# Optimization experiments

Hardware: AMD Instinct MI355X
Metric: run time of the kernel (lower is better)

Reference implementation:

```python
import jax, jax.numpy as jnp
import numpy as np

B, S, HIDDEN = 2, 4096, 4096
NUM_HEADS = 32
QK_NOPE = 128
QK_ROPE = 64
QK_HEAD = QK_NOPE + QK_ROPE
KV_LORA = 512
Q_LORA = 1536


def setup_inputs() -> dict:
    key = jax.random.key(0)
    k1, k2, k3, k4, k5, k6 = jax.random.split(key, 6)
    x = jax.random.normal(k1, (B, S, HIDDEN), dtype=jnp.float32)
    cos = jax.random.uniform(k2, (B, S, QK_ROPE), dtype=jnp.float32)
    sin = jax.random.uniform(k3, (B, S, QK_ROPE), dtype=jnp.float32)
    # Linear weights, torch layout [out, in]
    Wqa = jax.random.normal(k4, (Q_LORA, HIDDEN), dtype=jnp.float32) * 0.02
    Wqb = jax.random.normal(k5, (NUM_HEADS * QK_HEAD, Q_LORA), dtype=jnp.float32) * 0.02
    Wkva = jax.random.normal(k6, (KV_LORA + QK_ROPE, HIDDEN), dtype=jnp.float32) * 0.02
    return {"x": x, "cos": cos, "sin": sin, "Wqa": Wqa, "Wqb": Wqb, "Wkva": Wkva}


def _rotate_half(t):
    d = t.shape[-1] // 2
    return jnp.concatenate([-t[..., d:], t[..., :d]], axis=-1)


def reference(x, cos, sin, Wqa, Wqb, Wkva):
    b, s, _ = x.shape
    # low-rank Q: x -> q_lora -> heads*(nope+rope)
    q = jnp.einsum('bsh,rh->bsr', x, Wqa)
    q = jnp.einsum('bsr,or->bso', q, Wqb).reshape(b, s, NUM_HEADS, QK_HEAD)
    q_nope = q[..., :QK_NOPE]
    q_pe = q[..., QK_NOPE:]
    # KV down-projection with MQA rope part
    kv = jnp.einsum('bsh,oh->bso', x, Wkva)
    compressed_kv = kv[..., :KV_LORA]                         # [b,s,kv_lora]
    k_pe = kv[..., KV_LORA:].reshape(b, s, 1, QK_ROPE)
    # NeoX explicit RoPE, unsqueeze_dim=2
    c = cos[:, :, None, :]
    sn = sin[:, :, None, :]
    q_pe_rot = q_pe * c + _rotate_half(q_pe) * sn
    k_pe_rot = k_pe * c + _rotate_half(k_pe) * sn
    q_out = jnp.concatenate([q_nope, q_pe_rot], axis=-1).reshape(b, s, -1)
    k_out = k_pe_rot.reshape(b, s, QK_ROPE)
    return jnp.concatenate([q_out, k_out, compressed_kv], axis=-1)
```

## Files before the change

### kernel.cpp

```cpp
#include <hip/hip_runtime.h>
#include <hip/hip_bf16.h>
#include <stdint.h>

typedef __bf16 bf16x8 __attribute__((ext_vector_type(8)));
typedef float f32x4 __attribute__((ext_vector_type(4)));
typedef float fvec4 __attribute__((ext_vector_type(4)));
typedef unsigned short usvec4 __attribute__((ext_vector_type(4)));
typedef unsigned int ui32x4 __attribute__((ext_vector_type(4)));

#define AS3 __attribute__((address_space(3)))
#define AS1 __attribute__((address_space(1)))

static __device__ __forceinline__ unsigned short f2bf(float f) {
  unsigned int u = __float_as_uint(f);
  u += 0x7FFF + ((u >> 16) & 1);
  return (unsigned short)(u >> 16);
}


extern "C" __global__ void cvt_bf16_kernel(const float* __restrict__ src,
                                           unsigned short* __restrict__ dst,
                                           long n4) {
  long i = (long)blockIdx.x * blockDim.x + threadIdx.x;
  const long stride = (long)gridDim.x * blockDim.x;
  for (; i < n4; i += stride) {
    const fvec4 v = __builtin_nontemporal_load(&((const fvec4*)src)[i]);
    usvec4 o;
    o.x = f2bf(v.x); o.y = f2bf(v.y); o.z = f2bf(v.z); o.w = f2bf(v.w);
    ((usvec4*)dst)[i] = o;
  }
}

extern "C" __global__ void cvt_pad_kernel(const float* __restrict__ src,
                                          unsigned short* __restrict__ dst,
                                          long nsrc4, long ntot4) {
  long i = (long)blockIdx.x * blockDim.x + threadIdx.x;
  const long stride = (long)gridDim.x * blockDim.x;
  for (; i < ntot4; i += stride) {
    usvec4 o = {0, 0, 0, 0};
    if (i < nsrc4) {
      const fvec4 v = __builtin_nontemporal_load(&((const fvec4*)src)[i]);
      o.x = f2bf(v.x); o.y = f2bf(v.y); o.z = f2bf(v.z); o.w = f2bf(v.w);
    }
    ((usvec4*)dst)[i] = o;
  }
}

#define VMW(N) asm volatile("s_waitcnt vmcnt(" #N ")" ::: "memory")
#define BAR() do { __builtin_amdgcn_s_barrier(); \
                   __builtin_amdgcn_sched_barrier(0); } while (0)
#define LGKM0() do { asm volatile("s_waitcnt lgkmcnt(0)" ::: "memory"); \
                     __builtin_amdgcn_sched_barrier(0); } while (0)


template <int MODE>
__global__ __launch_bounds__(512, 2)
void mla_gemm(const __hip_bfloat16* __restrict__ A0p,
              const __hip_bfloat16* __restrict__ B0p, int K0,
              unsigned short* __restrict__ qlora,
              const float* __restrict__ cosp,
              const float* __restrict__ sinp,
              float* __restrict__ out) {
  extern __shared__ __align__(128) char lds[];
  const int tid = threadIdx.x;
  const int lane = tid & 63;
  const int w = tid >> 6;
  const int wm = w >> 2, wn = w & 3;
  const int l15 = lane & 15, lhi = lane >> 4;
  const int srow8 = lane >> 3;
  const int swzc = ((lane & 7) ^ srow8) * 8;

  const int bm = (int)blockIdx.x >> 3;
  const int bn = (int)blockIdx.x & 7;
  const __hip_bfloat16* Aptr = A0p;
  const __hip_bfloat16* Bptr = B0p;
  const int K = K0;
  const long brow = (long)bm * 256;
  const int bcol = bn * 256;

  const __hip_bfloat16* aSt = Aptr + (brow + w * 16 + srow8) * (long)K + swzc;
  const __hip_bfloat16* bSt = Bptr + ((long)bcol + srow8) * (long)K + swzc;
  const int wj0 = w * 16, wj1 = w * 16 + 8;
  const int cb_j0 = (2 * (wj0 >> 5)) * 32 + (wj0 & 31);
  const int cb_j1 = (2 * (wj1 >> 5)) * 32 + (wj1 & 31);
  const int ldsWj = w * 2048;

  const int aRdRow = (wm * 64 + l15) * 128;
  const int bRdRow = (wn * 32 + l15) * 128;
  const int ck0 = (lhi ^ (l15 & 7)) * 16;

  f32x4 acc[8][4] = {};
  bf16x8 aF[4][2];
  bf16x8 bF[2][2][2];

  const int T = K >> 6;

  auto stage = [&](int u, int kt) {
    const int b = kt & 1;
    if (u < 2) {
      const int off = b * 32768 + u * 16384 + ldsWj;
      __builtin_amdgcn_global_load_lds((AS1 void*)(aSt + (long)(u * 128) * K + kt * 64),
                                       (AS3 void*)(lds + off), 16, 0, 0);
      __builtin_amdgcn_global_load_lds((AS1 void*)(aSt + (long)(u * 128 + 8) * K + kt * 64),
                                       (AS3 void*)(lds + off + 1024), 16, 0, 0);
    } else {
      const int h = u - 2;
      const int off = 65536 + b * 32768 + h * 16384 + ldsWj;
      __builtin_amdgcn_global_load_lds((AS1 void*)(bSt + (long)(cb_j0 + h * 32) * K + kt * 64),
                                       (AS3 void*)(lds + off), 16, 0, 0);
      __builtin_amdgcn_global_load_lds((AS1 void*)(bSt + (long)(cb_j1 + h * 32) * K + kt * 64),
                                       (AS3 void*)(lds + off + 1024), 16, 0, 0);
    }
  };
  auto readA = [&](int qh, int b) {
    const int base = b * 32768 + qh * 16384 + aRdRow;
    #pragma unroll
    for (int fr = 0; fr < 4; ++fr) {
      aF[fr][0] = *(const bf16x8*)(lds + base + fr * 2048 + ck0);
      aF[fr][1] = *(const bf16x8*)(lds + base + fr * 2048 + (ck0 ^ 64));
    }
  };
  auto readB = [&](int c, int b) {
    const int base = 65536 + b * 32768 + c * 16384 + bRdRow;
    #pragma unroll
    for (int fq = 0; fq < 2; ++fq) {
      bF[c][fq][0] = *(const bf16x8*)(lds + base + fq * 2048 + ck0);
      bF[c][fq][1] = *(const bf16x8*)(lds + base + fq * 2048 + (ck0 ^ 64));
    }
  };
  auto mmac = [&](int qh, int c) {
    __builtin_amdgcn_s_setprio(1);
    #pragma unroll
    for (int fr = 0; fr < 4; ++fr)
      #pragma unroll
      for (int fq = 0; fq < 2; ++fq) {
        acc[qh * 4 + fr][c * 2 + fq] = __builtin_amdgcn_mfma_f32_16x16x32_bf16(
            aF[fr][0], bF[c][fq][0], acc[qh * 4 + fr][c * 2 + fq], 0, 0, 0);
        acc[qh * 4 + fr][c * 2 + fq] = __builtin_amdgcn_mfma_f32_16x16x32_bf16(
            aF[fr][1], bF[c][fq][1], acc[qh * 4 + fr][c * 2 + fq], 0, 0, 0);
      }
    __builtin_amdgcn_s_setprio(0);
  };

  stage(0, 0); stage(2, 0); stage(3, 0); stage(1, 0);
  stage(0, 1); stage(2, 1); stage(3, 1); stage(1, 1);
  VMW(12);
  BAR();

  for (int t = 0; t < T - 2; ++t) {
    const int b = t & 1;
    readA(0, b); readB(0, b); if (t) stage(1, t + 1);
    VMW(10); BAR(); LGKM0(); mmac(0, 0);
    readB(1, b);
    VMW(8); BAR(); LGKM0(); mmac(0, 1);
    readA(1, b); stage(0, t + 2); stage(2, t + 2);
    BAR(); LGKM0(); mmac(1, 1);
    stage(3, t + 2);
    VMW(10); BAR(); mmac(1, 0);
  }
  {
    const int b = (T - 2) & 1;
    readA(0, b); readB(0, b); stage(1, T - 1);
    VMW(10); BAR(); LGKM0(); mmac(0, 0);
    readB(1, b);
    VMW(8); BAR(); LGKM0(); mmac(0, 1);
    readA(1, b);
    BAR(); LGKM0(); mmac(1, 1);
    VMW(4); BAR(); mmac(1, 0);
  }
  {
    const int b = (T - 1) & 1;
    readA(0, b); readB(0, b);
    VMW(2); BAR(); LGKM0(); mmac(0, 0);
    readB(1, b);
    VMW(0); BAR(); LGKM0(); mmac(0, 1);
    readA(1, b);
    BAR(); LGKM0(); mmac(1, 1);
    BAR(); mmac(1, 0);
  }

  const int wcol = bcol + wn * 64;
  const long rbase = brow + wm * 64;
  char* eplds = lds + w * 4096;

  auto storeTileF32 = [&](int i8, float* dst) {
    #pragma unroll
    for (int j = 0; j < 4; ++j)
      #pragma unroll
      for (int r = 0; r < 4; ++r)
        *(float*)(eplds + (lhi * 4 + r) * 256 + ((j >> 1) * 32 + (j & 1) * 16 + l15) * 4) =
            acc[i8][j][r];
    asm volatile("s_waitcnt lgkmcnt(0)" ::: "memory");
    #pragma unroll
    for (int t = 0; t < 4; ++t) {
      const int r16 = t * 4 + (lane >> 4);
      const f32x4 v = *(const f32x4*)(eplds + r16 * 256 + (lane & 15) * 16);
      const long row = rbase + (i8 >> 2) * 128 + (i8 & 3) * 16 + r16;
      __builtin_nontemporal_store(v, (f32x4*)(dst + row * 6720 + (lane & 15) * 4));
    }
  };
  auto storeTileBf16 = [&](int i8) {
    #pragma unroll
    for (int j = 0; j < 4; ++j)
      #pragma unroll
      for (int r = 0; r < 4; ++r)
        *(unsigned short*)(eplds + (lhi * 4 + r) * 128 +
                           ((j >> 1) * 32 + (j & 1) * 16 + l15) * 2) = f2bf(acc[i8][j][r]);
    asm volatile("s_waitcnt lgkmcnt(0)" ::: "memory");
    #pragma unroll
    for (int t = 0; t < 2; ++t) {
      const int r16 = t * 8 + (lane >> 3);
      const ui32x4 v = *(const ui32x4*)(eplds + r16 * 128 + (lane & 7) * 16);
      const long row = rbase + (i8 >> 2) * 128 + (i8 & 3) * 16 + r16;
      *(ui32x4*)((char*)qlora + (row * 1536 + wcol) * 2 + (lane & 7) * 16) = v;
    }
  };

  if (wcol < 1536) {
    #pragma unroll
    for (int i8 = 0; i8 < 8; ++i8) storeTileBf16(i8);
  } else {
    #pragma unroll
    for (int i8 = 0; i8 < 8; ++i8) storeTileF32(i8, out + wcol + 4672);
  }
}


__global__ __launch_bounds__(512, 4)
void mla_gemm2(const __hip_bfloat16* __restrict__ Aq,
               const __hip_bfloat16* __restrict__ Bq,
               const __hip_bfloat16* __restrict__ Ak,
               const __hip_bfloat16* __restrict__ Bk,
               const float* __restrict__ cosp,
               const float* __restrict__ sinp,
               float* __restrict__ out) {
  extern __shared__ __align__(128) char lds[];
  const int tid = threadIdx.x;
  const int lane = tid & 63;
  const int w = tid >> 6;
  const int wm = w >> 1, wn = w & 1;
  const int l15 = lane & 15, lhi = lane >> 4;
  const int srow = lane >> 2;
  const int sslot = (lane & 3) ^ ((lane >> 3) & 3);

  const __hip_bfloat16* Ap;
  const __hip_bfloat16* Bp;
  int K, bm, bn;
  bool kpe;
  const int bid = (int)blockIdx.x;
  if (bid < 32) {
    kpe = true; bm = bid; bn = 0; Ap = Ak; Bp = Bk; K = 4096;
  } else {
    kpe = false;
    const int b2 = bid - 32;
    const int x = b2 & 7;
    const int i = b2 >> 3;
    const int r6 = i % 6;
    bm = i / 6;
    bn = x * 6 + r6;
    Ap = Aq; Bp = Bq; K = 1536;
  }
  const long brow = (long)bm * 256;
  const int bcol = bn * 128;

  const __hip_bfloat16* aSt = Ap + (brow + w * 16 + srow) * (long)K + sslot * 8;
  const __hip_bfloat16* bSt = Bp + ((long)bcol + w * 16 + srow) * (long)K + sslot * 8;

  const int kslot = (lhi ^ ((l15 >> 1) & 3)) * 16;
  const int aRd = (wm * 64 + l15) * 64 + kslot;
  const int bRd = 16384 + (wn * 64 + l15) * 64 + kslot;

  f32x4 acc[4][4] = {};
  const int T = K >> 5;

  auto stage = [&](int kt, int buf) {
    const int bo = buf * 24576;
    __builtin_amdgcn_global_load_lds((AS1 void*)(aSt + (long)kt * 32),
                                     (AS3 void*)(lds + bo + w * 1024), 16, 0, 0);
    __builtin_amdgcn_global_load_lds((AS1 void*)(aSt + 128L * K + (long)kt * 32),
                                     (AS3 void*)(lds + bo + 8192 + w * 1024), 16, 0, 0);
    __builtin_amdgcn_global_load_lds((AS1 void*)(bSt + (long)kt * 32),
                                     (AS3 void*)(lds + bo + 16384 + w * 1024), 16, 0, 0);
  };

  stage(0, 0); stage(1, 1);
  VMW(3);
  BAR();

  int cur = 0;
  for (int t = 0; t < T; ++t) {
    const int bo = cur * 24576;
    bf16x8 aF[4], bF[4];
    #pragma unroll
    for (int f = 0; f < 4; ++f)
      aF[f] = *(const bf16x8*)(lds + bo + aRd + f * 1024);
    #pragma unroll
    for (int f = 0; f < 4; ++f)
      bF[f] = *(const bf16x8*)(lds + bo + bRd + f * 1024);
    if (t + 2 < T) {
      int nx = cur + 2; if (nx >= 3) nx -= 3;
      stage(t + 2, nx);
      VMW(3);
    } else if (t + 2 == T) {
      VMW(0);
    }
    LGKM0();
    if (t < T - 1) BAR();
    __builtin_amdgcn_s_setprio(1);
    #pragma unroll
    for (int fr = 0; fr < 4; ++fr)
      #pragma unroll
      for (int fc = 0; fc < 4; ++fc)
        acc[fr][fc] = __builtin_amdgcn_mfma_f32_16x16x32_bf16(
            aF[fr], bF[fc], acc[fr][fc], 0, 0, 0);
    __builtin_amdgcn_s_setprio(0);
    cur = cur + 1; if (cur == 3) cur = 0;
  }

  const int wcol = bcol + wn * 64;
  const long rbase = brow + wm * 64;
  char* eplds = lds + w * 4096;

  auto storeT = [&](int fr, int colBase, bool rope) {
    #pragma unroll
    for (int fc = 0; fc < 4; ++fc)
      #pragma unroll
      for (int r = 0; r < 4; ++r) {
        float v = acc[fr][fc][r];
        if (rope) {
          const long row = rbase + fr * 16 + lhi * 4 + r;
          const int d = fc * 16 + l15;
          const float rot = (fc < 2) ? -acc[fr][fc + 2][r] : acc[fr][fc - 2][r];
          v = v * cosp[row * 64 + d] + rot * sinp[row * 64 + d];
        }
        *(float*)(eplds + (lhi * 4 + r) * 256 + (fc * 16 + l15) * 4) = v;
      }
    asm volatile("s_waitcnt lgkmcnt(0)" ::: "memory");
    #pragma unroll
    for (int tt = 0; tt < 4; ++tt) {
      const int r16 = tt * 4 + (lane >> 4);
      const f32x4 vv = *(const f32x4*)(eplds + r16 * 256 + (lane & 15) * 16);
      const long row = rbase + fr * 16 + r16;
      __builtin_nontemporal_store(vv,
          (f32x4*)(out + row * 6720 + colBase + (lane & 15) * 4));
    }
  };

  if (kpe) {
    if (wn == 0) {
      #pragma unroll
      for (int fr = 0; fr < 4; ++fr) storeT(fr, 6144, true);
    }
  } else if ((wcol % 192) == 128) {
    #pragma unroll
    for (int fr = 0; fr < 4; ++fr) storeT(fr, wcol, true);
  } else {
    #pragma unroll
    for (int fr = 0; fr < 4; ++fr) storeT(fr, wcol, false);
  }
}


extern "C" void kernel_launch(void* const* d_in, const int* in_sizes, int n_in,
                              void* d_out, int out_size, void* d_ws, size_t ws_size,
                              hipStream_t stream) {
  const float* x    = (const float*)d_in[0];
  const float* cosp = (const float*)d_in[1];
  const float* sinp = (const float*)d_in[2];
  const float* Wqa  = (const float*)d_in[3];
  const float* Wqb  = (const float*)d_in[4];
  const float* Wkva = (const float*)d_in[5];
  float* out = (float*)d_out;

  char* ws = (char*)d_ws;
  __hip_bfloat16* xb  = (__hip_bfloat16*)ws;
  __hip_bfloat16* w1  = (__hip_bfloat16*)(ws + 67108864L);
  __hip_bfloat16* wqb = (__hip_bfloat16*)(ws + 67108864L + 17825792L);
  unsigned short* ql  = (unsigned short*)(ws + 67108864L + 17825792L + 18874368L);

  cvt_bf16_kernel<<<2048, 256, 0, stream>>>(x,   (unsigned short*)xb,  8192L * 4096 / 4);
  cvt_bf16_kernel<<<1024, 256, 0, stream>>>(Wqa, (unsigned short*)w1,  1536L * 4096 / 4);
  cvt_pad_kernel<<<640, 256, 0, stream>>>(Wkva, (unsigned short*)(w1 + 1536L * 4096),
                                          576L * 4096 / 4, 640L * 4096 / 4);
  cvt_bf16_kernel<<<1024, 256, 0, stream>>>(Wqb, (unsigned short*)wqb, 6144L * 1536 / 4);

  (void)hipFuncSetAttribute((const void*)&mla_gemm<0>,
                            hipFuncAttributeMaxDynamicSharedMemorySize, 131072);
  (void)hipFuncSetAttribute((const void*)&mla_gemm2,
                            hipFuncAttributeMaxDynamicSharedMemorySize, 73728);

  mla_gemm<0><<<dim3(256), 512, 131072, stream>>>(xb, w1, 4096, ql, cosp, sinp, out);
  mla_gemm2<<<dim3(1568), 512, 73728, stream>>>((const __hip_bfloat16*)ql, wqb,
                                                xb, w1 + 2048L * 4096,
                                                cosp, sinp, out);
}
```

Measured before the change: 355.3 us.

## Load B operand directly from global into registers in second GEMM

The second GEMM kernel stops staging the B (weight) tile through LDS. Each wave now loads its B fragments straight from global memory into registers, double-buffered across two register sets, while A keeps its 3-stage LDS pipeline. This cuts the LDS footprint from 72KB to 48KB, which may allow more blocks per CU, and removes the LDS round trip for B. In exchange, B reads are no longer coalesced or shared between waves that use the same columns, and more registers are live.

```diff
diff --git a/kernel.cpp b/kernel.cpp
--- a/kernel.cpp
+++ b/kernel.cpp
@@ -264,59 +264,77 @@
   const int bcol = bn * 128;
 
   const __hip_bfloat16* aSt = Ap + (brow + w * 16 + srow) * (long)K + sslot * 8;
-  const __hip_bfloat16* bSt = Bp + ((long)bcol + w * 16 + srow) * (long)K + sslot * 8;
+  const __hip_bfloat16* bGl = Bp + ((long)bcol + wn * 64 + l15) * K + lhi * 8;
 
   const int kslot = (lhi ^ ((l15 >> 1) & 3)) * 16;
   const int aRd = (wm * 64 + l15) * 64 + kslot;
-  const int bRd = 16384 + (wn * 64 + l15) * 64 + kslot;
 
   f32x4 acc[4][4] = {};
+  bf16x8 aF[4];
+  bf16x8 bFa[4], bFb[4];
   const int T = K >> 5;
-
-  auto stage = [&](int kt, int buf) {
-    const int bo = buf * 24576;
+  const long fK16 = 16L * K;
+
+  auto stageA = [&](int kt, int buf) {
+    const int bo = buf * 16384;
     __builtin_amdgcn_global_load_lds((AS1 void*)(aSt + (long)kt * 32),
                                      (AS3 void*)(lds + bo + w * 1024), 16, 0, 0);
     __builtin_amdgcn_global_load_lds((AS1 void*)(aSt + 128L * K + (long)kt * 32),
                                      (AS3 void*)(lds + bo + 8192 + w * 1024), 16, 0, 0);
-    __builtin_amdgcn_global_load_lds((AS1 void*)(bSt + (long)kt * 32),
-                                     (AS3 void*)(lds + bo + 16384 + w * 1024), 16, 0, 0);
-  };
-
-  stage(0, 0); stage(1, 1);
-  VMW(3);
-  BAR();
-
-  int cur = 0;
-  for (int t = 0; t < T; ++t) {
-    const int bo = cur * 24576;
-    bf16x8 aF[4], bF[4];
+  };
+  auto loadB = [&](int kt, bf16x8* dst) {
+    const __hip_bfloat16* p = bGl + (long)kt * 32;
+    #pragma unroll
+    for (int fc = 0; fc < 4; ++fc)
+      dst[fc] = *(const bf16x8*)(p + fc * fK16);
+  };
+  auto readA = [&](int buf) {
+    const int bo = buf * 16384;
     #pragma unroll
     for (int f = 0; f < 4; ++f)
       aF[f] = *(const bf16x8*)(lds + bo + aRd + f * 1024);
-    #pragma unroll
-    for (int f = 0; f < 4; ++f)
-      bF[f] = *(const bf16x8*)(lds + bo + bRd + f * 1024);
-    if (t + 2 < T) {
-      int nx = cur + 2; if (nx >= 3) nx -= 3;
-      stage(t + 2, nx);
-      VMW(3);
-    } else if (t + 2 == T) {
-      VMW(0);
-    }
-    LGKM0();
-    if (t < T - 1) BAR();
+  };
+  auto mmac = [&](const bf16x8* bf) {
     __builtin_amdgcn_s_setprio(1);
     #pragma unroll
     for (int fr = 0; fr < 4; ++fr)
       #pragma unroll
       for (int fc = 0; fc < 4; ++fc)
         acc[fr][fc] = __builtin_amdgcn_mfma_f32_16x16x32_bf16(
-            aF[fr], bF[fc], acc[fr][fc], 0, 0, 0);
+            aF[fr], bf[fc], acc[fr][fc], 0, 0, 0);
     __builtin_amdgcn_s_setprio(0);
+  };
+
+  stageA(0, 0); stageA(1, 1);
+  loadB(0, bFa);
+  VMW(6);
+  BAR();
+
+  int cur = 0;
+  for (int t = 0; t < T - 2; t += 2) {
+    readA(cur);
+    loadB(t + 1, bFb);
+    { int nx = cur + 2; if (nx >= 3) nx -= 3; stageA(t + 2, nx); }
+    VMW(6); BAR(); LGKM0();
+    mmac(bFa);
     cur = cur + 1; if (cur == 3) cur = 0;
-  }
-
+    readA(cur);
+    loadB(t + 2, bFa);
+    if (t + 3 < T) { int nx = cur + 2; if (nx >= 3) nx -= 3; stageA(t + 3, nx); }
+    VMW(6); BAR(); LGKM0();
+    mmac(bFb);
+    cur = cur + 1; if (cur == 3) cur = 0;
+  }
+  readA(cur);
+  loadB(T - 1, bFb);
+  VMW(4); BAR(); LGKM0();
+  mmac(bFa);
+  cur = cur + 1; if (cur == 3) cur = 0;
+  readA(cur);
+  VMW(0); LGKM0();
+  mmac(bFb);
+
+  BAR();
   const int wcol = bcol + wn * 64;
   const long rbase = brow + wm * 64;
   char* eplds = lds + w * 4096;
@@ -387,10 +405,10 @@
   (void)hipFuncSetAttribute((const void*)&mla_gemm<0>,
                             hipFuncAttributeMaxDynamicSharedMemorySize, 131072);
   (void)hipFuncSetAttribute((const void*)&mla_gemm2,
-                            hipFuncAttributeMaxDynamicSharedMemorySize, 73728);
+                            hipFuncAttributeMaxDynamicSharedMemorySize, 49152);
 
   mla_gemm<0><<<dim3(256), 512, 131072, stream>>>(xb, w1, 4096, ql, cosp, sinp, out);
-  mla_gemm2<<<dim3(1568), 512, 73728, stream>>>((const __hip_bfloat16*)ql, wqb,
+  mla_gemm2<<<dim3(1568), 512, 49152, stream>>>((const __hip_bfloat16*)ql, wqb,
                                                 xb, w1 + 2048L * 4096,
                                                 cosp, sinp, out);
 }
```

New measurement: 676.7 us. +90.4%, slower.

## Add MODE 1 big-tile GEMM path with fused RoPE and swizzled block order

Applied to the files above, without the earlier changes.

Adds a grouped block-index swizzle to the first GEMM so that consecutive blocks share A/B tiles in L2. Also adds a MODE 1 variant of the 256x256 GEMM that would handle the Q up-projection plus the KV rope tail, applying RoPE in the epilogue. The launch code still calls only mla_gemm2 for the second stage, so MODE 1 is compiled but never launched. The swizzle in MODE 0 is the only change that runs.

```diff
diff --git a/kernel.cpp b/kernel.cpp
--- a/kernel.cpp
+++ b/kernel.cpp
@@ -57,6 +57,8 @@
 __global__ __launch_bounds__(512, 2)
 void mla_gemm(const __hip_bfloat16* __restrict__ A0p,
               const __hip_bfloat16* __restrict__ B0p, int K0,
+              const __hip_bfloat16* __restrict__ A1p,
+              const __hip_bfloat16* __restrict__ B1p,
               unsigned short* __restrict__ qlora,
               const float* __restrict__ cosp,
               const float* __restrict__ sinp,
@@ -70,11 +72,25 @@
   const int srow8 = lane >> 3;
   const int swzc = ((lane & 7) ^ srow8) * 8;
 
-  const int bm = (int)blockIdx.x >> 3;
-  const int bn = (int)blockIdx.x & 7;
-  const __hip_bfloat16* Aptr = A0p;
-  const __hip_bfloat16* Bptr = B0p;
-  const int K = K0;
+  const __hip_bfloat16* Aptr;
+  const __hip_bfloat16* Bptr;
+  int K, bm, bn;
+  bool isA2 = false;
+  if constexpr (MODE == 0) {
+    const int swz = ((int)blockIdx.x & 7) * 32 + ((int)blockIdx.x >> 3);
+    bm = swz >> 3; bn = swz & 7;
+    Aptr = A0p; Bptr = B0p; K = K0;
+  } else {
+    const int bid = (int)blockIdx.x;
+    if (bid < 32) {
+      isA2 = true; bm = bid; bn = 8; Aptr = A1p; Bptr = B1p; K = 4096;
+    } else {
+      const int b2 = bid - 32;
+      const int swz = (b2 & 7) * 96 + (b2 >> 3);
+      bm = swz / 24; bn = swz - bm * 24;
+      Aptr = A0p; Bptr = B0p; K = K0;
+    }
+  }
   const long brow = (long)bm * 256;
   const int bcol = bn * 256;
 
@@ -183,13 +199,20 @@
   const long rbase = brow + wm * 64;
   char* eplds = lds + w * 4096;
 
-  auto storeTileF32 = [&](int i8, float* dst) {
+  auto storeTileF32 = [&](int i8, float* dst, bool rope) {
     #pragma unroll
     for (int j = 0; j < 4; ++j)
       #pragma unroll
-      for (int r = 0; r < 4; ++r)
-        *(float*)(eplds + (lhi * 4 + r) * 256 + ((j >> 1) * 32 + (j & 1) * 16 + l15) * 4) =
-            acc[i8][j][r];
+      for (int r = 0; r < 4; ++r) {
+        float v = acc[i8][j][r];
+        if (rope) {
+          const long row = rbase + (i8 >> 2) * 128 + (i8 & 3) * 16 + lhi * 4 + r;
+          const int d = (j >> 1) * 32 + (j & 1) * 16 + l15;
+          const float rot = (j < 2) ? -acc[i8][j + 2][r] : acc[i8][j - 2][r];
+          v = v * cosp[row * 64 + d] + rot * sinp[row * 64 + d];
+        }
+        *(float*)(eplds + (lhi * 4 + r) * 256 + ((j >> 1) * 32 + (j & 1) * 16 + l15) * 4) = v;
+      }
     asm volatile("s_waitcnt lgkmcnt(0)" ::: "memory");
     #pragma unroll
     for (int t = 0; t < 4; ++t) {
@@ -216,12 +239,27 @@
     }
   };
 
-  if (wcol < 1536) {
-    #pragma unroll
-    for (int i8 = 0; i8 < 8; ++i8) storeTileBf16(i8);
+  if constexpr (MODE == 0) {
+    if (wcol < 1536) {
+      #pragma unroll
+      for (int i8 = 0; i8 < 8; ++i8) storeTileBf16(i8);
+    } else {
+      #pragma unroll
+      for (int i8 = 0; i8 < 8; ++i8) storeTileF32(i8, out + wcol + 4672, false);
+    }
   } else {
-    #pragma unroll
-    for (int i8 = 0; i8 < 8; ++i8) storeTileF32(i8, out + wcol + 4672);
+    if (isA2) {
+      if (wn == 0) {
+        #pragma unroll
+        for (int i8 = 0; i8 < 8; ++i8) storeTileF32(i8, out + 6144, true);
+      }
+    } else if ((wcol % 192) != 128) {
+      #pragma unroll
+      for (int i8 = 0; i8 < 8; ++i8) storeTileF32(i8, out + wcol, false);
+    } else {
+      #pragma unroll
+      for (int i8 = 0; i8 < 8; ++i8) storeTileF32(i8, out + wcol, true);
+    }
   }
 }
 
@@ -386,10 +424,13 @@
 
   (void)hipFuncSetAttribute((const void*)&mla_gemm<0>,
                             hipFuncAttributeMaxDynamicSharedMemorySize, 131072);
+  (void)hipFuncSetAttribute((const void*)&mla_gemm<1>,
+                            hipFuncAttributeMaxDynamicSharedMemorySize, 131072);
   (void)hipFuncSetAttribute((const void*)&mla_gemm2,
                             hipFuncAttributeMaxDynamicSharedMemorySize, 73728);
 
-  mla_gemm<0><<<dim3(256), 512, 131072, stream>>>(xb, w1, 4096, ql, cosp, sinp, out);
+  mla_gemm<0><<<dim3(256), 512, 131072, stream>>>(xb, w1, 4096, nullptr, nullptr,
+                                                  ql, cosp, sinp, out);
   mla_gemm2<<<dim3(1568), 512, 73728, stream>>>((const __hip_bfloat16*)ql, wqb,
                                                 xb, w1 + 2048L * 4096,
                                                 cosp, sinp, out);
```

Result: no change. 348.6 us (-1.9%).
